# Performance work log

Measured on AMD Instinct MI355X. Metric: run time of the kernel, lower is better.

Reference implementation:

```python
import jax, jax.numpy as jnp
import numpy as np

EPS = 1e-12  # torch F.normalize clamp_min eps

def _l2_normalize(x):
    n = jnp.linalg.norm(x, axis=-1, keepdims=True)
    return x / jnp.maximum(n, EPS)

def setup_inputs() -> dict:
    key = jax.random.key(0)
    k1, k2 = jax.random.split(key)
    z_e = jax.random.normal(k1, (32, 256, 32, 32), dtype=jnp.float32)
    weight = jax.random.normal(k2, (1024, 256), dtype=jnp.float32)
    return {"z_e": z_e, "weight": weight}

def reference(z_e, weight):
    B, C, H, W = z_e.shape  # C == embedding_dim
    z = jnp.transpose(z_e, (0, 2, 3, 1))            # [B,H,W,C]
    flat = _l2_normalize(z.reshape(-1, C))          # [N,C]
    w_n = _l2_normalize(weight)                     # [K,C]
    # distances = 2 - 2 * <flat, w_n>; computed without grad in original
    dist = 2.0 - 2.0 * jnp.matmul(flat, w_n.T)      # [N,K]
    idx = jnp.argmin(dist, axis=1)                  # [N]
    z_q = w_n[idx].reshape(B, H, W, C)              # gather codebook rows
    z_q = jnp.transpose(z_q, (0, 3, 1, 2))          # [B,C,H,W]
    indices = idx.reshape(B, H, W)
    return z_q, indices
```

## Files before the change

kernel.cpp:

```cpp
#include <hip/hip_runtime.h>


typedef _Float16 half8 __attribute__((ext_vector_type(8)));
typedef float    floatx4 __attribute__((ext_vector_type(4)));

#define C_DIM 256
#define K_CODES 1024
#define HW 1024
#define NPIX 32768
#define NTILES 8

__global__ __launch_bounds__(256) void vq_prep(
        const float* __restrict__ z, const float* __restrict__ w,
        float* __restrict__ w_n, _Float16* __restrict__ wfh, _Float16* __restrict__ wfl,
        _Float16* __restrict__ zfh, _Float16* __restrict__ zfl) {
    __shared__ float wsum[4];
    __shared__ unsigned pk[64][257];
    const int t = threadIdx.x;

    if (blockIdx.x < K_CODES) {
        const int c = blockIdx.x;
        float x = w[c * C_DIM + t];
        float s = x * x;
        #pragma unroll
        for (int off = 32; off > 0; off >>= 1) s += __shfl_down(s, off, 64);
        if ((t & 63) == 0) wsum[t >> 6] = s;
        __syncthreads();
        float tot = wsum[0] + wsum[1] + wsum[2] + wsum[3];
        float inv = 1.0f / fmaxf(sqrtf(tot), 1e-12f);
        float y = x * inv;
        w_n[c * C_DIM + t] = y;
        float ys = 16.0f * y;
        _Float16 hi = (_Float16)ys;
        _Float16 lo = (_Float16)(ys - (float)hi);
        const int kt = t >> 5, l = ((t >> 3) & 3) * 16 + (c & 15), j = t & 7;
        const size_t fo = ((size_t)(c >> 6) * 8 + kt) * 2048 + ((c >> 4) & 3) * 512
                        + l * 8 + j;
        wfh[fo] = hi;
        wfl[fo] = lo;
        return;
    }

    const int zb = blockIdx.x - K_CODES;
    const int pg = zb * 64;
    const int b  = pg >> 10, p0 = pg & 1023;
    const float* zp = z + (size_t)b * C_DIM * HW + p0;

    const int cc = t >> 4, pp = (t & 15) * 4;
    #pragma unroll
    for (int it = 0; it < 16; it++) {
        const int c = it * 16 + cc;
        floatx4 v = *(const floatx4*)(zp + (size_t)c * HW + pp);
        #pragma unroll
        for (int j = 0; j < 4; j++) {
            float xs = 4.0f * v[j];
            _Float16 h = (_Float16)xs;
            _Float16 l = (_Float16)(xs - (float)h);
            pk[pp + j][c] = (unsigned)__builtin_bit_cast(unsigned short, h)
                          | ((unsigned)__builtin_bit_cast(unsigned short, l) << 16);
        }
    }
    __syncthreads();

    const int u = t >> 6, l = t & 63;
    const int row = u * 16 + (l & 15);
    #pragma unroll
    for (int kt = 0; kt < 8; kt++) {
        half8 hv, lv;
        #pragma unroll
        for (int j = 0; j < 8; j++) {
            unsigned v = pk[row][kt * 32 + (l >> 4) * 8 + j];
            hv[j] = __builtin_bit_cast(_Float16, (unsigned short)(v & 0xffffu));
            lv[j] = __builtin_bit_cast(_Float16, (unsigned short)(v >> 16));
        }
        const size_t fo = ((size_t)zb * 8 + kt) * 2048 + u * 512 + l * 8;
        *(half8*)(zfh + fo) = hv;
        *(half8*)(zfl + fo) = lv;
    }
}

__global__ __launch_bounds__(256, 2) void vq_gemm(
        const _Float16* __restrict__ zfh, const _Float16* __restrict__ zfl,
        const _Float16* __restrict__ wfh, const _Float16* __restrict__ wfl,
        float* __restrict__ cand_val, int* __restrict__ cand_idx) {
    __shared__ float red_v[128][2];
    __shared__ int   red_i[128][2];

    const int tid  = threadIdx.x;
    const int lane = tid & 63, wave = tid >> 6;
    const int wm = wave >> 1, wn = wave & 1;
    const int quad = lane >> 4, l15 = lane & 15;
    const int m0 = blockIdx.x * 128, n0 = blockIdx.y * 128;

    const size_t aoff = (size_t)(blockIdx.x * 2 + wm) * 8 * 2048 + lane * 8;
    const size_t boff = (size_t)(blockIdx.y * 2 + wn) * 8 * 2048 + lane * 8;
    const _Float16* pAh = zfh + aoff;
    const _Float16* pAl = zfl + aoff;
    const _Float16* pBh = wfh + boff;
    const _Float16* pBl = wfl + boff;

    floatx4 acc[4][4];
    #pragma unroll
    for (int i = 0; i < 4; i++)
        #pragma unroll
        for (int j = 0; j < 4; j++) acc[i][j] = (floatx4){0.f, 0.f, 0.f, 0.f};

    half8 A0h[4], A0l[4], B0h[4], B0l[4];
    half8 A1h[4], A1l[4], B1h[4], B1l[4];

#define LOADK(AH, AL, BH, BL, kt)                                              \
    {   _Pragma("unroll")                                                      \
        for (int i = 0; i < 4; i++) {                                          \
            AH[i] = *(const half8*)(pAh + (kt) * 2048 + i * 512);              \
            AL[i] = *(const half8*)(pAl + (kt) * 2048 + i * 512);              \
            BH[i] = *(const half8*)(pBh + (kt) * 2048 + i * 512);              \
            BL[i] = *(const half8*)(pBl + (kt) * 2048 + i * 512);              \
        }                                                                      \
    }

#define MFMAK(AH, AL, BH, BL)                                                  \
    {   _Pragma("unroll")                                                      \
        for (int mi = 0; mi < 4; mi++)                                         \
            _Pragma("unroll")                                                  \
            for (int ni = 0; ni < 4; ni++) {                                   \
                acc[mi][ni] = __builtin_amdgcn_mfma_f32_16x16x32_f16(          \
                    AH[mi], BH[ni], acc[mi][ni], 0, 0, 0);                     \
                acc[mi][ni] = __builtin_amdgcn_mfma_f32_16x16x32_f16(          \
                    AH[mi], BL[ni], acc[mi][ni], 0, 0, 0);                     \
                acc[mi][ni] = __builtin_amdgcn_mfma_f32_16x16x32_f16(          \
                    AL[mi], BH[ni], acc[mi][ni], 0, 0, 0);                     \
            }                                                                  \
    }

    LOADK(A0h, A0l, B0h, B0l, 0);
    LOADK(A1h, A1l, B1h, B1l, 1);  MFMAK(A0h, A0l, B0h, B0l);
    LOADK(A0h, A0l, B0h, B0l, 2);  MFMAK(A1h, A1l, B1h, B1l);
    LOADK(A1h, A1l, B1h, B1l, 3);  MFMAK(A0h, A0l, B0h, B0l);
    LOADK(A0h, A0l, B0h, B0l, 4);  MFMAK(A1h, A1l, B1h, B1l);
    LOADK(A1h, A1l, B1h, B1l, 5);  MFMAK(A0h, A0l, B0h, B0l);
    LOADK(A0h, A0l, B0h, B0l, 6);  MFMAK(A1h, A1l, B1h, B1l);
    LOADK(A1h, A1l, B1h, B1l, 7);  MFMAK(A0h, A0l, B0h, B0l);
                                   MFMAK(A1h, A1l, B1h, B1l);
#undef LOADK
#undef MFMAK

    #pragma unroll
    for (int mi = 0; mi < 4; mi++) {
        #pragma unroll
        for (int r = 0; r < 4; r++) {
            float bv = -__builtin_inff();
            int   bi = 0x7fffffff;
            #pragma unroll
            for (int ni = 0; ni < 4; ni++) {
                float v = acc[mi][ni][r];
                int  ci = n0 + wn * 64 + ni * 16 + l15;
                if (v > bv || (v == bv && ci < bi)) { bv = v; bi = ci; }
            }
            #pragma unroll
            for (int mk = 8; mk; mk >>= 1) {
                float ov = __shfl_xor(bv, mk, 16);
                int   oi = __shfl_xor(bi, mk, 16);
                if (ov > bv || (ov == bv && oi < bi)) { bv = ov; bi = oi; }
            }
            if (l15 == 0) {
                int row = wm * 64 + mi * 16 + quad * 4 + r;
                red_v[row][wn] = bv;
                red_i[row][wn] = bi;
            }
        }
    }
    __syncthreads();
    if (tid < 128) {
        float bv = red_v[tid][0]; int bi = red_i[tid][0];
        float v2 = red_v[tid][1]; int i2 = red_i[tid][1];
        if (v2 > bv || (v2 == bv && i2 < bi)) { bv = v2; bi = i2; }
        const int pix = m0 + tid;
        cand_val[(size_t)pix * NTILES + blockIdx.y] = bv;
        cand_idx[(size_t)pix * NTILES + blockIdx.y] = bi;
    }
}

__global__ __launch_bounds__(256) void vq_finalize(
        const float* __restrict__ cand_val,
        const int*   __restrict__ cand_idx,
        const float* __restrict__ w_n,
        float* __restrict__ zq,
        float* __restrict__ idx_out) {
    __shared__ float tile[64][257];
    __shared__ int   idx_s[64];
    const int t    = threadIdx.x;
    const int lane = t & 63, wave = t >> 6;
    const int n0   = blockIdx.x * 64;
    const int b    = n0 >> 10, p0 = n0 & 1023;

    if (t < 64) {
        const int n = n0 + t;
        const size_t base = (size_t)n * NTILES;
        float bv = cand_val[base]; int bi = cand_idx[base];
        #pragma unroll
        for (int j = 1; j < NTILES; j++) {
            float v = cand_val[base + j];
            int   c = cand_idx[base + j];
            if (v > bv || (v == bv && c < bi)) { bv = v; bi = c; }
        }
        idx_s[t] = bi;
        idx_out[n] = (float)bi;
    }
    __syncthreads();
    #pragma unroll
    for (int i = 0; i < 16; i++) {
        const int p = wave * 16 + i;
        const int row = idx_s[p];
        floatx4 v = *(const floatx4*)(w_n + (size_t)row * C_DIM + lane * 4);
        *(floatx4*)&tile[p][lane * 4] = v;
    }
    __syncthreads();
    float* zqb = zq + (size_t)b * (C_DIM * HW) + p0;
    #pragma unroll
    for (int it = 0; it < 16; it++) {
        const int c = it * 16 + wave * 4 + (lane >> 4);
        const int p = (lane & 15) * 4;
        floatx4 v = { tile[p][c], tile[p + 1][c], tile[p + 2][c], tile[p + 3][c] };
        *(floatx4*)(zqb + (size_t)c * HW + p) = v;
    }
}

extern "C" void kernel_launch(void* const* d_in, const int* in_sizes, int n_in,
                              void* d_out, int out_size, void* d_ws, size_t ws_size,
                              hipStream_t stream) {
    const float* z = (const float*)d_in[0];
    const float* w = (const float*)d_in[1];
    float* out     = (float*)d_out;

    char* ws = (char*)d_ws;
    _Float16* zfh  = (_Float16*)(ws);
    _Float16* zfl  = (_Float16*)(ws + (16u << 20));
    float*    w_n  = (float*)(ws + (32u << 20));
    _Float16* wfh  = (_Float16*)(ws + (33u << 20));
    _Float16* wfl  = (_Float16*)(ws + (33u << 20) + (1u << 19));
    float*    cval = (float*)(ws + (34u << 20));
    int*      cidx = (int*)(ws + (35u << 20));

    vq_prep<<<K_CODES + NPIX / 64, 256, 0, stream>>>(z, w, w_n, wfh, wfl, zfh, zfl);
    vq_gemm<<<dim3(NPIX / 128, NTILES), 256, 0, stream>>>(zfh, zfl, wfh, wfl, cval, cidx);
    vq_finalize<<<NPIX / 64, 256, 0, stream>>>(cval, cidx, w_n, out, out + 8388608);
}
```

Baseline: 161.1 us.

## Fuse codebook GEMM, argmin and gather into one kernel per 64-pixel tile

```diff
diff --git a/kernel.cpp b/kernel.cpp
--- a/kernel.cpp
+++ b/kernel.cpp
@@ -8,7 +8,10 @@
 #define K_CODES 1024
 #define HW 1024
 #define NPIX 32768
-#define NTILES 8
+
+#define GLOAD_LDS16(g, l) __builtin_amdgcn_global_load_lds(                    \
+    (const __attribute__((address_space(1))) unsigned int*)(g),                \
+    (__attribute__((address_space(3))) unsigned int*)(l), 16, 0, 0)
 
 __global__ __launch_bounds__(256) void vq_prep(
         const float* __restrict__ z, const float* __restrict__ w,
@@ -79,149 +82,124 @@
     }
 }
 
-__global__ __launch_bounds__(256, 2) void vq_gemm(
+__global__ __launch_bounds__(256, 2) void vq_gemm_fused(
         const _Float16* __restrict__ zfh, const _Float16* __restrict__ zfl,
         const _Float16* __restrict__ wfh, const _Float16* __restrict__ wfl,
-        float* __restrict__ cand_val, int* __restrict__ cand_idx) {
-    __shared__ float red_v[128][2];
-    __shared__ int   red_i[128][2];
+        const float* __restrict__ w_n,
+        float* __restrict__ zq, float* __restrict__ idx_out) {
+    __shared__ float tile[64][257];
+    __shared__ float red_v[64][16];
+    __shared__ int   red_i[64][16];
+    __shared__ int   idx_s[64];
+    _Float16* Ah = (_Float16*)&tile[0][0];
+    _Float16* Al = Ah + 16384;
 
     const int tid  = threadIdx.x;
     const int lane = tid & 63, wave = tid >> 6;
-    const int wm = wave >> 1, wn = wave & 1;
     const int quad = lane >> 4, l15 = lane & 15;
-    const int m0 = blockIdx.x * 128, n0 = blockIdx.y * 128;
-
-    const size_t aoff = (size_t)(blockIdx.x * 2 + wm) * 8 * 2048 + lane * 8;
-    const size_t boff = (size_t)(blockIdx.y * 2 + wn) * 8 * 2048 + lane * 8;
-    const _Float16* pAh = zfh + aoff;
-    const _Float16* pAl = zfl + aoff;
-    const _Float16* pBh = wfh + boff;
-    const _Float16* pBl = wfl + boff;
-
-    floatx4 acc[4][4];
-    #pragma unroll
-    for (int i = 0; i < 4; i++)
-        #pragma unroll
-        for (int j = 0; j < 4; j++) acc[i][j] = (floatx4){0.f, 0.f, 0.f, 0.f};
-
-    half8 A0h[4], A0l[4], B0h[4], B0l[4];
-    half8 A1h[4], A1l[4], B1h[4], B1l[4];
-
-#define LOADK(AH, AL, BH, BL, kt)                                              \
-    {   _Pragma("unroll")                                                      \
-        for (int i = 0; i < 4; i++) {                                          \
-            AH[i] = *(const half8*)(pAh + (kt) * 2048 + i * 512);              \
-            AL[i] = *(const half8*)(pAl + (kt) * 2048 + i * 512);              \
-            BH[i] = *(const half8*)(pBh + (kt) * 2048 + i * 512);              \
-            BL[i] = *(const half8*)(pBl + (kt) * 2048 + i * 512);              \
-        }                                                                      \
-    }
-
-#define MFMAK(AH, AL, BH, BL)                                                  \
-    {   _Pragma("unroll")                                                      \
-        for (int mi = 0; mi < 4; mi++)                                         \
-            _Pragma("unroll")                                                  \
-            for (int ni = 0; ni < 4; ni++) {                                   \
-                acc[mi][ni] = __builtin_amdgcn_mfma_f32_16x16x32_f16(          \
-                    AH[mi], BH[ni], acc[mi][ni], 0, 0, 0);                     \
-                acc[mi][ni] = __builtin_amdgcn_mfma_f32_16x16x32_f16(          \
-                    AH[mi], BL[ni], acc[mi][ni], 0, 0, 0);                     \
-                acc[mi][ni] = __builtin_amdgcn_mfma_f32_16x16x32_f16(          \
-                    AL[mi], BH[ni], acc[mi][ni], 0, 0, 0);                     \
-            }                                                                  \
-    }
-
-    LOADK(A0h, A0l, B0h, B0l, 0);
-    LOADK(A1h, A1l, B1h, B1l, 1);  MFMAK(A0h, A0l, B0h, B0l);
-    LOADK(A0h, A0l, B0h, B0l, 2);  MFMAK(A1h, A1l, B1h, B1l);
-    LOADK(A1h, A1l, B1h, B1l, 3);  MFMAK(A0h, A0l, B0h, B0l);
-    LOADK(A0h, A0l, B0h, B0l, 4);  MFMAK(A1h, A1l, B1h, B1l);
-    LOADK(A1h, A1l, B1h, B1l, 5);  MFMAK(A0h, A0l, B0h, B0l);
-    LOADK(A0h, A0l, B0h, B0l, 6);  MFMAK(A1h, A1l, B1h, B1l);
-    LOADK(A1h, A1l, B1h, B1l, 7);  MFMAK(A0h, A0l, B0h, B0l);
-                                   MFMAK(A1h, A1l, B1h, B1l);
-#undef LOADK
-#undef MFMAK
-
-    #pragma unroll
-    for (int mi = 0; mi < 4; mi++) {
-        #pragma unroll
-        for (int r = 0; r < 4; r++) {
-            float bv = -__builtin_inff();
-            int   bi = 0x7fffffff;
-            #pragma unroll
-            for (int ni = 0; ni < 4; ni++) {
-                float v = acc[mi][ni][r];
-                int  ci = n0 + wn * 64 + ni * 16 + l15;
-                if (v > bv || (v == bv && ci < bi)) { bv = v; bi = ci; }
+    const int g4   = blockIdx.x;
+
+    {
+        const _Float16* gh = zfh + (size_t)g4 * 16384 + lane * 8;
+        const _Float16* gl = zfl + (size_t)g4 * 16384 + lane * 8;
+        #pragma unroll
+        for (int i = 0; i < 8; i++) {
+            const int c = wave * 8 + i;
+            GLOAD_LDS16(gh + c * 512, Ah + c * 512);
+            GLOAD_LDS16(gl + c * 512, Al + c * 512);
+        }
+    }
+    __syncthreads();
+    for (int p = 0; p < 4; p++) {
+        const int g4w = p * 4 + wave;
+        const int cb  = g4w * 64;
+        const _Float16* pBh = wfh + (size_t)g4w * 16384 + lane * 8;
+        const _Float16* pBl = wfl + (size_t)g4w * 16384 + lane * 8;
+
+        floatx4 acc[4][4];
+        #pragma unroll
+        for (int i = 0; i < 4; i++)
+            #pragma unroll
+            for (int j = 0; j < 4; j++) acc[i][j] = (floatx4){0.f, 0.f, 0.f, 0.f};
+
+        for (int kt = 0; kt < 8; kt++) {
+            half8 bh[4], bl[4], ah[4], al[4];
+            #pragma unroll
+            for (int i = 0; i < 4; i++) {
+                bh[i] = *(const half8*)(pBh + kt * 2048 + i * 512);
+                bl[i] = *(const half8*)(pBl + kt * 2048 + i * 512);
+                ah[i] = *(const half8*)&Ah[kt * 2048 + i * 512 + lane * 8];
+                al[i] = *(const half8*)&Al[kt * 2048 + i * 512 + lane * 8];
             }
-            #pragma unroll
-            for (int mk = 8; mk; mk >>= 1) {
-                float ov = __shfl_xor(bv, mk, 16);
-                int   oi = __shfl_xor(bi, mk, 16);
-                if (ov > bv || (ov == bv && oi < bi)) { bv = ov; bi = oi; }
+            __builtin_amdgcn_s_setprio(1);
+            #pragma unroll
+            for (int mi = 0; mi < 4; mi++)
+                #pragma unroll
+                for (int ni = 0; ni < 4; ni++) {
+                    acc[mi][ni] = __builtin_amdgcn_mfma_f32_16x16x32_f16(ah[mi], bh[ni], acc[mi][ni], 0, 0, 0);
+                    acc[mi][ni] = __builtin_amdgcn_mfma_f32_16x16x32_f16(ah[mi], bl[ni], acc[mi][ni], 0, 0, 0);
+                    acc[mi][ni] = __builtin_amdgcn_mfma_f32_16x16x32_f16(al[mi], bh[ni], acc[mi][ni], 0, 0, 0);
+                }
+            __builtin_amdgcn_s_setprio(0);
+        }
+
+        #pragma unroll
+        for (int mi = 0; mi < 4; mi++) {
+            #pragma unroll
+            for (int r = 0; r < 4; r++) {
+                float bv = -__builtin_inff();
+                int   bi = 0x7fffffff;
+                #pragma unroll
+                for (int ni = 0; ni < 4; ni++) {
+                    float v = acc[mi][ni][r];
+                    int  ci = cb + ni * 16 + l15;
+                    if (v > bv || (v == bv && ci < bi)) { bv = v; bi = ci; }
+                }
+                #pragma unroll
+                for (int mk = 8; mk; mk >>= 1) {
+                    float ov = __shfl_xor(bv, mk, 16);
+                    int   oi = __shfl_xor(bi, mk, 16);
+                    if (ov > bv || (ov == bv && oi < bi)) { bv = ov; bi = oi; }
+                }
+                if (l15 == 0) {
+                    int row = mi * 16 + quad * 4 + r;
+                    red_v[row][g4w] = bv;
+                    red_i[row][g4w] = bi;
+                }
             }
-            if (l15 == 0) {
-                int row = wm * 64 + mi * 16 + quad * 4 + r;
-                red_v[row][wn] = bv;
-                red_i[row][wn] = bi;
-            }
-        }
-    }
-    __syncthreads();
-    if (tid < 128) {
+        }
+    }
+    __syncthreads();
+
+    if (tid < 64) {
         float bv = red_v[tid][0]; int bi = red_i[tid][0];
-        float v2 = red_v[tid][1]; int i2 = red_i[tid][1];
-        if (v2 > bv || (v2 == bv && i2 < bi)) { bv = v2; bi = i2; }
-        const int pix = m0 + tid;
-        cand_val[(size_t)pix * NTILES + blockIdx.y] = bv;
-        cand_idx[(size_t)pix * NTILES + blockIdx.y] = bi;
-    }
-}
-
-__global__ __launch_bounds__(256) void vq_finalize(
-        const float* __restrict__ cand_val,
-        const int*   __restrict__ cand_idx,
-        const float* __restrict__ w_n,
-        float* __restrict__ zq,
-        float* __restrict__ idx_out) {
-    __shared__ float tile[64][257];
-    __shared__ int   idx_s[64];
-    const int t    = threadIdx.x;
-    const int lane = t & 63, wave = t >> 6;
-    const int n0   = blockIdx.x * 64;
-    const int b    = n0 >> 10, p0 = n0 & 1023;
-
-    if (t < 64) {
-        const int n = n0 + t;
-        const size_t base = (size_t)n * NTILES;
-        float bv = cand_val[base]; int bi = cand_idx[base];
-        #pragma unroll
-        for (int j = 1; j < NTILES; j++) {
-            float v = cand_val[base + j];
-            int   c = cand_idx[base + j];
+        #pragma unroll
+        for (int e = 1; e < 16; e++) {
+            float v = red_v[tid][e];
+            int   c = red_i[tid][e];
             if (v > bv || (v == bv && c < bi)) { bv = v; bi = c; }
         }
-        idx_s[t] = bi;
-        idx_out[n] = (float)bi;
-    }
-    __syncthreads();
+        idx_s[tid] = bi;
+        idx_out[g4 * 64 + tid] = (float)bi;
+    }
+    __syncthreads();
+
     #pragma unroll
     for (int i = 0; i < 16; i++) {
-        const int p = wave * 16 + i;
-        const int row = idx_s[p];
+        const int px = wave * 16 + i;
+        const int row = idx_s[px];
         floatx4 v = *(const floatx4*)(w_n + (size_t)row * C_DIM + lane * 4);
-        *(floatx4*)&tile[p][lane * 4] = v;
-    }
-    __syncthreads();
-    float* zqb = zq + (size_t)b * (C_DIM * HW) + p0;
+        *(floatx4*)&tile[px][lane * 4] = v;
+    }
+    __syncthreads();
+    const int n0 = g4 * 64, bb = n0 >> 10, p0 = n0 & 1023;
+    float* zqb = zq + (size_t)bb * (C_DIM * HW) + p0;
     #pragma unroll
     for (int it = 0; it < 16; it++) {
         const int c = it * 16 + wave * 4 + (lane >> 4);
-        const int p = (lane & 15) * 4;
-        floatx4 v = { tile[p][c], tile[p + 1][c], tile[p + 2][c], tile[p + 3][c] };
-        *(floatx4*)(zqb + (size_t)c * HW + p) = v;
+        const int px = (lane & 15) * 4;
+        floatx4 v = { tile[px][c], tile[px + 1][c], tile[px + 2][c], tile[px + 3][c] };
+        *(floatx4*)(zqb + (size_t)c * HW + px) = v;
     }
 }
 
@@ -238,10 +216,8 @@
     float*    w_n  = (float*)(ws + (32u << 20));
     _Float16* wfh  = (_Float16*)(ws + (33u << 20));
     _Float16* wfl  = (_Float16*)(ws + (33u << 20) + (1u << 19));
-    float*    cval = (float*)(ws + (34u << 20));
-    int*      cidx = (int*)(ws + (35u << 20));
 
     vq_prep<<<K_CODES + NPIX / 64, 256, 0, stream>>>(z, w, w_n, wfh, wfl, zfh, zfl);
-    vq_gemm<<<dim3(NPIX / 128, NTILES), 256, 0, stream>>>(zfh, zfl, wfh, wfl, cval, cidx);
-    vq_finalize<<<NPIX / 64, 256, 0, stream>>>(cval, cidx, w_n, out, out + 8388608);
+    vq_gemm_fused<<<NPIX / 64, 256, 0, stream>>>(zfh, zfl, wfh, wfl, w_n,
+                                                 out, out + 8388608);
 }
```

Result: slower. 201.0 us (+24.8%).
